# Kernel optimization log

Measured on AMD Instinct MI355X. Metric: run time of the kernel, lower is better.

## Reference

```python
import jax, jax.numpy as jnp
import numpy as np

B, N_HEADS, F_TOK = 8, 12, 768
GRID_H, GRID_W = 32, 32
N_TOK = 1 + GRID_H * GRID_W  # 1025 (readout token + patches)
F_HEAD = F_TOK // N_HEADS    # 64
NUM_DIST = (2 * GRID_H - 1) * (2 * GRID_W - 1) + 3  # 3972


def _build_relpos_index(gh, gw):
    # BEiT-style relative position index with 3 extra slots for the readout token
    coords = np.stack(np.meshgrid(np.arange(gh), np.arange(gw), indexing='ij'))  # (2, gh, gw)
    flat = coords.reshape(2, -1)                                                 # (2, gh*gw)
    rel = flat[:, :, None] - flat[:, None, :]                                    # (2, P, P)
    rel = rel.transpose(1, 2, 0).astype(np.int64)                                # (P, P, 2)
    rel[:, :, 0] += gh - 1
    rel[:, :, 1] += gw - 1
    rel[:, :, 0] *= 2 * gw - 1
    rpi = rel.sum(-1)                                                            # (P, P)
    n = 1 + gh * gw
    nd = (2 * gh - 1) * (2 * gw - 1) + 3
    idx = np.zeros((n, n), dtype=np.int32)
    idx[1:, 1:] = rpi
    idx[0, :] = nd - 3  # readout -> all
    idx[:, 0] = nd - 2  # all -> readout
    idx[0, 0] = nd - 1  # readout -> readout
    return idx


def setup_inputs() -> dict:
    key = jax.random.key(0)
    ks = jax.random.split(key, 7)
    tokens = jax.random.normal(ks[0], (B, N_TOK, F_TOK), dtype=jnp.float32)
    qkv_w = jax.random.normal(ks[1], (3 * F_TOK, F_TOK), dtype=jnp.float32) * 0.02
    q_bias = jax.random.normal(ks[2], (1, N_HEADS, 1, F_HEAD), dtype=jnp.float32) * 0.02
    v_bias = jax.random.normal(ks[3], (1, N_HEADS, 1, F_HEAD), dtype=jnp.float32) * 0.02
    relpos_table = jax.random.normal(ks[4], (NUM_DIST, N_HEADS), dtype=jnp.float32) * 0.02
    proj_w = jax.random.normal(ks[5], (F_TOK, F_TOK), dtype=jnp.float32) * 0.02
    proj_b = jax.random.normal(ks[6], (F_TOK,), dtype=jnp.float32) * 0.02
    relpos_index = jnp.asarray(_build_relpos_index(GRID_H, GRID_W))  # (N, N) int32
    return {
        'tokens': tokens, 'qkv_w': qkv_w, 'q_bias': q_bias, 'v_bias': v_bias,
        'relpos_table': relpos_table, 'proj_w': proj_w, 'proj_b': proj_b,
        'relpos_index': relpos_index, 'patch_h': GRID_H, 'patch_w': GRID_W,
    }


def reference(tokens, qkv_w, q_bias, v_bias, relpos_table, proj_w, proj_b,
              relpos_index, patch_h, patch_w):
    b, n, f_tok = tokens.shape
    # qkv projection (no bias): (B, N, 3F) -> (3, B, H, N, f)
    qkv = tokens @ qkv_w.T
    qkv = qkv.reshape(b, n, 3, N_HEADS, F_HEAD).transpose(2, 0, 3, 1, 4)
    q, k, v = qkv[0], qkv[1], qkv[2]
    q = (q + q_bias) * (F_HEAD ** -0.5)
    v = v + v_bias
    # attention scores: (B, H, N, N)
    attn = jnp.einsum('bhnf,bhmf->bhnm', q, k)
    # relative position bias gather: (N, N, H) -> (H, N, N)
    bias = relpos_table[relpos_index].transpose(2, 0, 1)
    attn = attn + bias[None]
    w = jax.nn.softmax(attn, axis=-1)
    out = jnp.einsum('bhnm,bhmf->bhnf', w, v)
    out = out.transpose(0, 2, 1, 3).reshape(b, n, N_HEADS * F_HEAD)
    return out @ proj_w.T + proj_b
```

## Files before the change

### kernel.cpp

```cpp
#include <hip/hip_runtime.h>

#define B_ 8
#define NH 12
#define NTOK 1025
#define FT 768
#define MROWS (B_*NTOK)
#define QPAD 1025
#define CH2 34
#define NQT 36
#define NTT 34
#define NDIST 3972
#define LOG2E 1.44269504089f

typedef __bf16 bf16x8 __attribute__((ext_vector_type(8)));
typedef __bf16 bf16x2 __attribute__((ext_vector_type(2)));
typedef float floatx4 __attribute__((ext_vector_type(4)));
typedef float floatx16 __attribute__((ext_vector_type(16)));
typedef int intx4 __attribute__((ext_vector_type(4)));

__device__ __forceinline__ void async_ld16(const void* gp, void* lp) {
  __builtin_amdgcn_global_load_lds(
      (const __attribute__((address_space(1))) void*)gp,
      (__attribute__((address_space(3))) void*)lp, 16, 0, 0);
}

__global__ __launch_bounds__(256) void cvt_bf16(const float* __restrict__ src,
                                                __bf16* __restrict__ dst, int n4) {
  int i = blockIdx.x * 256 + threadIdx.x;
  if (i >= n4) return;
  float4 v = ((const float4*)src)[i];
  __bf16 o[4] = {(__bf16)v.x, (__bf16)v.y, (__bf16)v.z, (__bf16)v.w};
  *(uint2*)(dst + 4 * (size_t)i) = *(uint2*)o;
}

__global__ __launch_bounds__(256) void table_prep(const float* __restrict__ table,
                                                  __bf16* __restrict__ tableT) {
  int i = blockIdx.x * 256 + threadIdx.x;
  if (i >= NH * NDIST) return;
  int h = i / NDIST, d = i - h * NDIST;
  tableT[i] = (__bf16)(table[(size_t)d * NH + h] * LOG2E);
}

__global__ __launch_bounds__(256) void bias_gather_t(
    const int* __restrict__ idx, const __bf16* __restrict__ tableT,
    __bf16* __restrict__ Bb) {
  __shared__ int ids_l[32][33];
  const int qt = blockIdx.x, tt = blockIdx.y;
  const int t = threadIdx.x;
  {
    const int row = t >> 3, c4 = (t & 7) * 4;
    int qrow = qt * 32 + row; if (qrow > NTOK - 1) qrow = NTOK - 1;
    const int* src = idx + (size_t)qrow * NTOK;
#pragma unroll
    for (int j = 0; j < 4; ++j) {
      int token = tt * 32 + c4 + j; if (token > NTOK - 1) token = NTOK - 1;
      ids_l[row][c4 + j] = src[token];
    }
  }
  __syncthreads();
  const int lane = t & 63, w = t >> 6;
  const int l31 = lane & 31, hb = lane >> 5;
  int ids[16]; bool ok[16];
#pragma unroll
  for (int j = 0; j < 16; ++j) {
    const int col = (j & 3) + 8 * (j >> 2) + 4 * hb;
    ok[j] = tt * 32 + col < NTOK;
    ids[j] = ids_l[l31][col];
  }
#pragma unroll
  for (int g = 0; g < 3; ++g) {
    const int h = w + g * 4;
    const __bf16* tb = tableT + (size_t)h * NDIST;
    __bf16 v[16] __attribute__((aligned(16)));
#pragma unroll
    for (int j = 0; j < 16; ++j)
      v[j] = ok[j] ? tb[ids[j]] : (__bf16)(-1e30f);
    uint4* dst = (uint4*)(Bb + (((size_t)h * NQT + qt) * NTT + tt) * 1024 + lane * 16);
    dst[0] = ((uint4*)v)[0];
    dst[1] = ((uint4*)v)[1];
  }
}

__device__ __forceinline__ void gemm256_pipe(
    const __bf16* __restrict__ A, const __bf16* __restrict__ W,
    int am0, int n0, __bf16* Lt, floatx4 acc[4][4]) {
  const int tid = threadIdx.x, wave = tid >> 6, lane = tid & 63;
  const int l = lane & 15, qd = lane >> 4;
  const int srow = lane >> 2, sg = lane & 3;
  const int swb = (sg ^ (srow & 3)) * 8;
  const int wr = wave >> 1, wc = wave & 1;

  const __bf16* gsrc[3];
  int gdst[3];
#pragma unroll
  for (int i = 0; i < 3; ++i) {
    const int g = wave * 3 + i;
    if (g < 16) {
      int row = am0 + g * 16 + srow; if (row > MROWS - 1) row = MROWS - 1;
      gsrc[i] = A + (size_t)row * FT + swb;
      gdst[i] = g * 512;
    } else {
      const int row = n0 + (g - 16) * 16 + srow;
      gsrc[i] = W + (size_t)row * FT + swb;
      gdst[i] = 8192 + (g - 16) * 512;
    }
  }
  const int fsw = (qd ^ (l & 3)) * 8;

  auto issue = [&](int k, int buf) {
    __bf16* base = Lt + buf * 12288;
#pragma unroll
    for (int i = 0; i < 3; ++i)
      async_ld16(gsrc[i] + k * 32, base + gdst[i]);
  };
  auto step = [&](int buf) {
    __builtin_amdgcn_s_barrier();
    const __bf16* ab = Lt + buf * 12288;
    const __bf16* bb = ab + 8192;
    bf16x8 aF[4], bF[4];
#pragma unroll
    for (int t = 0; t < 4; ++t)
      aF[t] = *(const bf16x8*)(ab + (wr * 64 + t * 16 + l) * 32 + fsw);
#pragma unroll
    for (int u = 0; u < 4; ++u)
      bF[u] = *(const bf16x8*)(bb + (wc * 64 + u * 16 + l) * 32 + fsw);
#pragma unroll
    for (int t = 0; t < 4; ++t)
#pragma unroll
      for (int u = 0; u < 4; ++u)
        acc[t][u] = __builtin_amdgcn_mfma_f32_16x16x32_bf16(aF[t], bF[u], acc[t][u], 0, 0, 0);
  };

  issue(0, 0);
  int b0 = 0;
  for (int k = 0; k < 24; ++k) {
    if (k < 23) {
      int b1 = b0 + 1; if (b1 == 3) b1 = 0;
      issue(k + 1, b1);
      __builtin_amdgcn_s_waitcnt(0x0F73);
    } else {
      __builtin_amdgcn_s_waitcnt(0x0F70);
    }
    step(b0);
    ++b0; if (b0 == 3) b0 = 0;
  }
}

__global__ __launch_bounds__(512, 4) void qkv_gemm256(
    const __bf16* __restrict__ tokens, const __bf16* __restrict__ qkvw,
    const float* __restrict__ qbias, const float* __restrict__ vbias,
    __bf16* __restrict__ Qb, __bf16* __restrict__ Kc, __bf16* __restrict__ Vc) {
  __shared__ __bf16 Lt[3 * 12288];
  const int u0 = blockIdx.x;
  const int c = u0 & 7, i0 = u0 >> 3;
  const int base = (c < 2) ? c * 75 : 150 + (c - 2) * 74;
  const int w = base + i0;
  const int mt = w / 18, ni = w % 18;
  const int am0 = mt * 256, n0 = ni * 128;
  const int tid = threadIdx.x, wave = tid >> 6, lane = tid & 63;
  const int l = lane & 15, qd = lane >> 4;
  const int wr = wave >> 1, wc = wave & 1;
  floatx4 acc[4][4];
#pragma unroll
  for (int t = 0; t < 4; ++t)
#pragma unroll
    for (int u = 0; u < 4; ++u) acc[t][u] = (floatx4){0.f, 0.f, 0.f, 0.f};
  gemm256_pipe(tokens, qkvw, am0, n0, Lt, acc);

  const int which = ni / 6;
  const int nrem0 = (ni - which * 6) * 128;
#pragma unroll
  for (int u = 0; u < 4; ++u) {
    const int rem = nrem0 + wc * 64 + u * 16 + l;
    const int h = rem >> 6, f = rem & 63;
    const float qb = (which == 0) ? qbias[h * 64 + f] : 0.f;
    const float vb = (which == 2) ? vbias[h * 64 + f] : 0.f;
#pragma unroll
    for (int t = 0; t < 4; ++t) {
      const int gmb = am0 + wr * 64 + t * 16 + qd * 4;
#pragma unroll
      for (int r = 0; r < 4; ++r) {
        const int gm = gmb + r;
        if (gm >= MROWS) continue;
        const int b = (int)(((unsigned)gm * 16369u) >> 24);
        const int tok = gm - b * 1025;
        const size_t bh = (size_t)(b * NH + h);
        const float v = acc[t][u][r];
        if (which == 0) {
          Qb[(bh * QPAD + tok) * 64 + f] = (__bf16)((v + qb) * (0.125f * LOG2E));
        } else if (which == 1) {
          const size_t e = (bh * CH2 + (tok >> 5)) * 2048 +
                           (f >> 3) * 256 + (tok & 31) * 8 + (f & 7);
          Kc[e] = (__bf16)v;
        } else {
          const size_t e = (bh * CH2 + (tok >> 5)) * 2048 +
                           (((tok >> 3) & 3) * 64 + f) * 8 + (tok & 7);
          Vc[e] = (__bf16)(v + vb);
        }
      }
    }
  }
}

__global__ __launch_bounds__(512, 4) void proj_gemm256(
    const __bf16* __restrict__ Ao, const __bf16* __restrict__ projw,
    const float* __restrict__ projb, float* __restrict__ out) {
  __shared__ __bf16 Lt[3 * 12288];
  const int u0 = blockIdx.x;
  const int c = u0 & 7, i0 = u0 >> 3;
  const int base = (c < 6) ? c * 25 : 150 + (c - 6) * 24;
  const int w = base + i0;
  const int mt = w / 6, ni = w % 6;
  const int am0 = mt * 256, n0 = ni * 128;
  const int tid = threadIdx.x, wave = tid >> 6, lane = tid & 63;
  const int l = lane & 15, qd = lane >> 4;
  const int wr = wave >> 1, wc = wave & 1;
  floatx4 acc[4][4];
#pragma unroll
  for (int t = 0; t < 4; ++t)
#pragma unroll
    for (int u = 0; u < 4; ++u) acc[t][u] = (floatx4){0.f, 0.f, 0.f, 0.f};
  gemm256_pipe(Ao, projw, am0, n0, Lt, acc);

#pragma unroll
  for (int u = 0; u < 4; ++u) {
    const int gn = n0 + wc * 64 + u * 16 + l;
    const float pb = projb[gn];
#pragma unroll
    for (int t = 0; t < 4; ++t) {
      const int gmb = am0 + wr * 64 + t * 16 + qd * 4;
#pragma unroll
      for (int r = 0; r < 4; ++r) {
        const int gm = gmb + r;
        if (gm < MROWS) out[(size_t)gm * FT + gn] = acc[t][u][r] + pb;
      }
    }
  }
}

__global__ __launch_bounds__(256) void attn_flash(
    const __bf16* __restrict__ Qb, const __bf16* __restrict__ Kc,
    const __bf16* __restrict__ Vc, const __bf16* __restrict__ Bb,
    __bf16* __restrict__ Ao) {
  __shared__ __bf16 Kl[5][2048], Vl[5][2048];
  const int bh = blockIdx.x;
  const int h = bh % NH, b = bh / NH;
  const int wave = threadIdx.x >> 6, lane = threadIdx.x & 63;
  const int l31 = lane & 31, hb = lane >> 5;
  const int qt = blockIdx.y * 4 + wave;
  int qrow = qt * 32 + l31; if (qrow > NTOK - 1) qrow = NTOK - 1;

  bf16x8 qf[4];
  {
    const __bf16* Qp = Qb + ((size_t)bh * QPAD + qrow) * 64 + hb * 8;
#pragma unroll
    for (int d = 0; d < 4; ++d) qf[d] = *(const bf16x8*)(Qp + d * 16);
  }

  floatx16 o0, o1;
#pragma unroll
  for (int j = 0; j < 16; ++j) { o0[j] = 0.f; o1[j] = 0.f; }
  float lsum = 0.f;

  const int sw = wave & 1;
  const __bf16* Sg = ((wave < 2) ? Kc : Vc) + (size_t)bh * CH2 * 2048 +
                     sw * 1024 + lane * 8;
  __bf16* Sl0 = ((wave < 2) ? &Kl[0][0] : &Vl[0][0]) + sw * 1024;
  const __bf16* Bg = Bb + ((size_t)h * NQT + qt) * NTT * 1024 + lane * 16;

  auto issueS = [&](int c, int buf) {
    const __bf16* src = Sg + (size_t)c * 2048;
    __bf16* dst = Sl0 + buf * 2048;
    async_ld16(src, dst);
    async_ld16(src + 512, dst + 512);
  };

  auto compute = [&](int buf, bf16x8 cb0, bf16x8 cb1) {
    const __bf16* Kb = &Kl[buf][0];
    const __bf16* Vb = &Vl[buf][0];
    floatx16 st;
#pragma unroll
    for (int j = 0; j < 16; ++j) st[j] = 0.f;
#pragma unroll
    for (int dk = 0; dk < 4; ++dk) {
      bf16x8 a = *(const bf16x8*)(Kb + ((dk * 2 + hb) * 32 + l31) * 8);
      st = __builtin_amdgcn_mfma_f32_32x32x16_bf16(a, qf[dk], st, 0, 0, 0);
    }
    float e[16];
#pragma unroll
    for (int j = 0; j < 16; ++j) {
      const float bj = (float)(j < 8 ? cb0[j] : cb1[j - 8]);
      e[j] = __builtin_amdgcn_exp2f(st[j] + bj);
      lsum += e[j];
    }
    int pk[8];
#pragma unroll
    for (int j2 = 0; j2 < 8; ++j2) {
      bf16x2 pr = {(__bf16)e[2 * j2], (__bf16)e[2 * j2 + 1]};
      pk[j2] = __builtin_bit_cast(int, pr);
    }
#pragma unroll
    for (int ks = 0; ks < 2; ++ks) {
      const int r01a = pk[4 * ks + 0], r01b = pk[4 * ks + 1];
      const int r23a = pk[4 * ks + 2], r23b = pk[4 * ks + 3];
      const int t01a = __shfl_xor(r01a, 32), t01b = __shfl_xor(r01b, 32);
      const int t23a = __shfl_xor(r23a, 32), t23b = __shfl_xor(r23b, 32);
      intx4 fi;
      fi[0] = hb ? t23a : r01a;
      fi[1] = hb ? t23b : r01b;
      fi[2] = hb ? r23a : t01a;
      fi[3] = hb ? r23b : t01b;
      bf16x8 pb = __builtin_bit_cast(bf16x8, fi);
      bf16x8 va0 = *(const bf16x8*)(Vb + ((ks * 2 + hb) * 64 + l31) * 8);
      bf16x8 va1 = *(const bf16x8*)(Vb + ((ks * 2 + hb) * 64 + 32 + l31) * 8);
      o0 = __builtin_amdgcn_mfma_f32_32x32x16_bf16(va0, pb, o0, 0, 0, 0);
      o1 = __builtin_amdgcn_mfma_f32_32x32x16_bf16(va1, pb, o1, 0, 0, 0);
    }
  };

  issueS(0, 0);
  bf16x8 bA0 = *(const bf16x8*)(Bg);
  bf16x8 bA1 = *(const bf16x8*)(Bg + 8);
  issueS(1, 1);
  bf16x8 bB0 = *(const bf16x8*)(Bg + 1024);
  bf16x8 bB1 = *(const bf16x8*)(Bg + 1024 + 8);
  issueS(2, 2);

  int bc = 0;
  for (int ci = 0; ci < 15; ++ci) {
    const int c = 2 * ci;
    __builtin_amdgcn_s_waitcnt(0x0F76);
    __builtin_amdgcn_s_barrier();
    compute(bc, bA0, bA1);
    bA0 = *(const bf16x8*)(Bg + (size_t)(c + 2) * 1024);
    bA1 = *(const bf16x8*)(Bg + (size_t)(c + 2) * 1024 + 8);
    { int b3 = bc + 3; if (b3 >= 5) b3 -= 5; issueS(c + 3, b3); }
    int bc1 = bc + 1; if (bc1 == 5) bc1 = 0;
    __builtin_amdgcn_s_waitcnt(0x0F76);
    __builtin_amdgcn_s_barrier();
    compute(bc1, bB0, bB1);
    bB0 = *(const bf16x8*)(Bg + (size_t)(c + 3) * 1024);
    bB1 = *(const bf16x8*)(Bg + (size_t)(c + 3) * 1024 + 8);
    { int b4 = bc + 4; if (b4 >= 5) b4 -= 5; issueS(c + 4, b4); }
    bc += 2; if (bc >= 5) bc -= 5;
  }
  __builtin_amdgcn_s_waitcnt(0x0F76);
  __builtin_amdgcn_s_barrier();
  compute(0, bA0, bA1);
  bA0 = *(const bf16x8*)(Bg + (size_t)32 * 1024);
  bA1 = *(const bf16x8*)(Bg + (size_t)32 * 1024 + 8);
  issueS(33, 3);
  __builtin_amdgcn_s_waitcnt(0x0F76);
  __builtin_amdgcn_s_barrier();
  compute(1, bB0, bB1);
  bB0 = *(const bf16x8*)(Bg + (size_t)33 * 1024);
  bB1 = *(const bf16x8*)(Bg + (size_t)33 * 1024 + 8);
  __builtin_amdgcn_s_waitcnt(0x0F74);
  __builtin_amdgcn_s_barrier();
  compute(2, bA0, bA1);
  __builtin_amdgcn_s_waitcnt(0x0F70);
  __builtin_amdgcn_s_barrier();
  compute(3, bB0, bB1);

  const float ltot = lsum + __shfl_xor(lsum, 32);
  const float rinv = 1.0f / ltot;
  const int tok = qt * 32 + l31;
  if (tok < NTOK) {
    __bf16* op = Ao + ((size_t)b * NTOK + tok) * FT + h * 64;
#pragma unroll
    for (int ft = 0; ft < 2; ++ft) {
#pragma unroll
      for (int jg = 0; jg < 4; ++jg) {
        const int f = ft * 32 + jg * 8 + hb * 4;
        __bf16 v4[4] __attribute__((aligned(8)));
#pragma unroll
        for (int q = 0; q < 4; ++q) {
          const float ov = ft ? o1[jg * 4 + q] : o0[jg * 4 + q];
          v4[q] = (__bf16)(ov * rinv);
        }
        *(uint2*)(op + f) = *(uint2*)v4;
      }
    }
  }
}

extern "C" void kernel_launch(void* const* d_in, const int* in_sizes, int n_in,
                              void* d_out, int out_size, void* d_ws, size_t ws_size,
                              hipStream_t stream) {
  (void)in_sizes; (void)n_in; (void)out_size; (void)ws_size;
  const float* tokens = (const float*)d_in[0];
  const float* qkvw   = (const float*)d_in[1];
  const float* qbias  = (const float*)d_in[2];
  const float* vbias  = (const float*)d_in[3];
  const float* table  = (const float*)d_in[4];
  const float* projw  = (const float*)d_in[5];
  const float* projb  = (const float*)d_in[6];
  const int*   rpidx  = (const int*)d_in[7];
  float* out = (float*)d_out;
  char* ws = (char*)d_ws;

  const size_t QBQ = (size_t)B_ * NH * QPAD * 64 * 2;
  const size_t KVB = (size_t)B_ * NH * CH2 * 2048 * 2;
  const size_t BBT = (size_t)NH * NQT * NTT * 1024 * 2;
  const size_t AOB = (size_t)MROWS * FT * 2;
  const size_t WQB = (size_t)3 * FT * FT * 2;
  const size_t WPB = (size_t)FT * FT * 2;
  __bf16* Qb = (__bf16*)(ws);
  __bf16* Kc = (__bf16*)(ws + QBQ);
  __bf16* Vc = (__bf16*)(ws + QBQ + KVB);
  __bf16* Bb = (__bf16*)(ws + QBQ + 2 * KVB);
  __bf16* Tb = (__bf16*)(ws + QBQ + 2 * KVB + BBT);
  __bf16* Ao = Tb;
  __bf16* Wq = (__bf16*)(ws + QBQ + 2 * KVB + BBT + AOB);
  __bf16* Wp = (__bf16*)(ws + QBQ + 2 * KVB + BBT + AOB + WQB);
  __bf16* Tt = (__bf16*)(ws + QBQ + 2 * KVB + BBT + AOB + WQB + WPB);

  cvt_bf16<<<(MROWS * FT / 4 + 255) / 256, 256, 0, stream>>>(tokens, Tb, MROWS * FT / 4);
  cvt_bf16<<<(3 * FT * FT / 4 + 255) / 256, 256, 0, stream>>>(qkvw, Wq, 3 * FT * FT / 4);
  cvt_bf16<<<(FT * FT / 4 + 255) / 256, 256, 0, stream>>>(projw, Wp, FT * FT / 4);
  table_prep<<<(NH * NDIST + 255) / 256, 256, 0, stream>>>(table, Tt);
  bias_gather_t<<<dim3(NQT, NTT), 256, 0, stream>>>(rpidx, Tt, Bb);
  qkv_gemm256<<<33 * 18, 512, 0, stream>>>(Tb, Wq, qbias, vbias, Qb, Kc, Vc);
  attn_flash<<<dim3(B_ * NH, 9), 256, 0, stream>>>(Qb, Kc, Vc, Bb, Ao);
  proj_gemm256<<<33 * 6, 512, 0, stream>>>(Ao, Wp, projb, out);
}
```

Measured before the change: 246.7 us.

## Process 64-key tiles per stage with triple buffering and split QK/SV phases

The attention loop now handles two 32-key tiles per pipeline stage, using a 3-deep LDS ring of 4096-element K/V buffers instead of a 5-deep ring of 2048-element buffers. The bias is folded into the MFMA accumulator init, prefetch is issued between the QK and PV phases, and s_setprio hints are wrapped around the MFMA sections. The aim is to halve the barrier count and interleave exp work with MFMA across waves. A launch-bounds occupancy hint of 3 blocks is added, which may constrain registers given the doubled score accumulators.

```diff
diff --git a/kernel.cpp b/kernel.cpp
--- a/kernel.cpp
+++ b/kernel.cpp
@@ -238,11 +238,11 @@
   }
 }
 
-__global__ __launch_bounds__(256) void attn_flash(
+__global__ __launch_bounds__(256, 3) void attn_flash(
     const __bf16* __restrict__ Qb, const __bf16* __restrict__ Kc,
     const __bf16* __restrict__ Vc, const __bf16* __restrict__ Bb,
     __bf16* __restrict__ Ao) {
-  __shared__ __bf16 Kl[5][2048], Vl[5][2048];
+  __shared__ __bf16 Kl[3][4096], Vl[3][4096];
   const int bh = blockIdx.x;
   const int h = bh % NH, b = bh / NH;
   const int wave = threadIdx.x >> 6, lane = threadIdx.x & 63;
@@ -260,109 +260,123 @@
   floatx16 o0, o1;
 #pragma unroll
   for (int j = 0; j < 16; ++j) { o0[j] = 0.f; o1[j] = 0.f; }
-  float lsum = 0.f;
+  float lsA = 0.f, lsB = 0.f;
 
   const int sw = wave & 1;
   const __bf16* Sg = ((wave < 2) ? Kc : Vc) + (size_t)bh * CH2 * 2048 +
-                     sw * 1024 + lane * 8;
-  __bf16* Sl0 = ((wave < 2) ? &Kl[0][0] : &Vl[0][0]) + sw * 1024;
+                     sw * 2048 + lane * 8;
+  __bf16* Sl0 = ((wave < 2) ? &Kl[0][0] : &Vl[0][0]) + sw * 2048;
   const __bf16* Bg = Bb + ((size_t)h * NQT + qt) * NTT * 1024 + lane * 16;
 
-  auto issueS = [&](int c, int buf) {
-    const __bf16* src = Sg + (size_t)c * 2048;
-    __bf16* dst = Sl0 + buf * 2048;
+  auto issueS = [&](int c2, int buf) {
+    const __bf16* src = Sg + (size_t)c2 * 4096;
+    __bf16* dst = Sl0 + buf * 4096;
     async_ld16(src, dst);
     async_ld16(src + 512, dst + 512);
-  };
-
-  auto compute = [&](int buf, bf16x8 cb0, bf16x8 cb1) {
+    async_ld16(src + 1024, dst + 1024);
+    async_ld16(src + 1536, dst + 1536);
+  };
+
+  bf16x8 bA0, bA1, bA2, bA3, bB0, bB1, bB2, bB3;
+  auto loadBA = [&](int c2) {
+    const __bf16* p = Bg + (size_t)(2 * c2) * 1024;
+    bA0 = *(const bf16x8*)(p);
+    bA1 = *(const bf16x8*)(p + 8);
+    bA2 = *(const bf16x8*)(p + 1024);
+    bA3 = *(const bf16x8*)(p + 1032);
+  };
+  auto loadBB = [&](int c2) {
+    const __bf16* p = Bg + (size_t)(2 * c2) * 1024;
+    bB0 = *(const bf16x8*)(p);
+    bB1 = *(const bf16x8*)(p + 8);
+    bB2 = *(const bf16x8*)(p + 1024);
+    bB3 = *(const bf16x8*)(p + 1032);
+  };
+
+  floatx16 st0, st1;
+  auto qkPart = [&](int buf, bf16x8 c0, bf16x8 c1, bf16x8 c2, bf16x8 c3) {
     const __bf16* Kb = &Kl[buf][0];
-    const __bf16* Vb = &Vl[buf][0];
-    floatx16 st;
-#pragma unroll
-    for (int j = 0; j < 16; ++j) st[j] = 0.f;
+#pragma unroll
+    for (int j = 0; j < 16; ++j) {
+      st0[j] = (float)(j < 8 ? c0[j] : c1[j - 8]);
+      st1[j] = (float)(j < 8 ? c2[j] : c3[j - 8]);
+    }
+    __builtin_amdgcn_s_setprio(1);
 #pragma unroll
     for (int dk = 0; dk < 4; ++dk) {
-      bf16x8 a = *(const bf16x8*)(Kb + ((dk * 2 + hb) * 32 + l31) * 8);
-      st = __builtin_amdgcn_mfma_f32_32x32x16_bf16(a, qf[dk], st, 0, 0, 0);
-    }
-    float e[16];
-#pragma unroll
-    for (int j = 0; j < 16; ++j) {
-      const float bj = (float)(j < 8 ? cb0[j] : cb1[j - 8]);
-      e[j] = __builtin_amdgcn_exp2f(st[j] + bj);
-      lsum += e[j];
-    }
-    int pk[8];
-#pragma unroll
-    for (int j2 = 0; j2 < 8; ++j2) {
-      bf16x2 pr = {(__bf16)e[2 * j2], (__bf16)e[2 * j2 + 1]};
-      pk[j2] = __builtin_bit_cast(int, pr);
-    }
-#pragma unroll
-    for (int ks = 0; ks < 2; ++ks) {
-      const int r01a = pk[4 * ks + 0], r01b = pk[4 * ks + 1];
-      const int r23a = pk[4 * ks + 2], r23b = pk[4 * ks + 3];
-      const int t01a = __shfl_xor(r01a, 32), t01b = __shfl_xor(r01b, 32);
-      const int t23a = __shfl_xor(r23a, 32), t23b = __shfl_xor(r23b, 32);
-      intx4 fi;
-      fi[0] = hb ? t23a : r01a;
-      fi[1] = hb ? t23b : r01b;
-      fi[2] = hb ? r23a : t01a;
-      fi[3] = hb ? r23b : t01b;
-      bf16x8 pb = __builtin_bit_cast(bf16x8, fi);
-      bf16x8 va0 = *(const bf16x8*)(Vb + ((ks * 2 + hb) * 64 + l31) * 8);
-      bf16x8 va1 = *(const bf16x8*)(Vb + ((ks * 2 + hb) * 64 + 32 + l31) * 8);
-      o0 = __builtin_amdgcn_mfma_f32_32x32x16_bf16(va0, pb, o0, 0, 0, 0);
-      o1 = __builtin_amdgcn_mfma_f32_32x32x16_bf16(va1, pb, o1, 0, 0, 0);
+      bf16x8 a0 = *(const bf16x8*)(Kb + ((dk * 2 + hb) * 32 + l31) * 8);
+      bf16x8 a1 = *(const bf16x8*)(Kb + 2048 + ((dk * 2 + hb) * 32 + l31) * 8);
+      st0 = __builtin_amdgcn_mfma_f32_32x32x16_bf16(a0, qf[dk], st0, 0, 0, 0);
+      st1 = __builtin_amdgcn_mfma_f32_32x32x16_bf16(a1, qf[dk], st1, 0, 0, 0);
+    }
+    __builtin_amdgcn_s_setprio(0);
+  };
+
+  auto svPart = [&](int buf) {
+#pragma unroll
+    for (int th = 0; th < 2; ++th) {
+      const floatx16& st = th ? st1 : st0;
+      const __bf16* Vb = &Vl[buf][0] + th * 2048;
+      float e[16];
+#pragma unroll
+      for (int j = 0; j < 16; ++j) e[j] = __builtin_amdgcn_exp2f(st[j]);
+      lsA += ((e[0] + e[1]) + (e[2] + e[3])) + ((e[4] + e[5]) + (e[6] + e[7]));
+      lsB += ((e[8] + e[9]) + (e[10] + e[11])) + ((e[12] + e[13]) + (e[14] + e[15]));
+      int pk[8];
+#pragma unroll
+      for (int j2 = 0; j2 < 8; ++j2) {
+        bf16x2 pr = {(__bf16)e[2 * j2], (__bf16)e[2 * j2 + 1]};
+        pk[j2] = __builtin_bit_cast(int, pr);
+      }
+      __builtin_amdgcn_s_setprio(1);
+#pragma unroll
+      for (int ks = 0; ks < 2; ++ks) {
+        const int r01a = pk[4 * ks + 0], r01b = pk[4 * ks + 1];
+        const int r23a = pk[4 * ks + 2], r23b = pk[4 * ks + 3];
+        const int t01a = __shfl_xor(r01a, 32), t01b = __shfl_xor(r01b, 32);
+        const int t23a = __shfl_xor(r23a, 32), t23b = __shfl_xor(r23b, 32);
+        intx4 fi;
+        fi[0] = hb ? t23a : r01a;
+        fi[1] = hb ? t23b : r01b;
+        fi[2] = hb ? r23a : t01a;
+        fi[3] = hb ? r23b : t01b;
+        bf16x8 pb = __builtin_bit_cast(bf16x8, fi);
+        bf16x8 va0 = *(const bf16x8*)(Vb + ((ks * 2 + hb) * 64 + l31) * 8);
+        bf16x8 va1 = *(const bf16x8*)(Vb + ((ks * 2 + hb) * 64 + 32 + l31) * 8);
+        o0 = __builtin_amdgcn_mfma_f32_32x32x16_bf16(va0, pb, o0, 0, 0, 0);
+        o1 = __builtin_amdgcn_mfma_f32_32x32x16_bf16(va1, pb, o1, 0, 0, 0);
+      }
+      __builtin_amdgcn_s_setprio(0);
     }
   };
 
   issueS(0, 0);
-  bf16x8 bA0 = *(const bf16x8*)(Bg);
-  bf16x8 bA1 = *(const bf16x8*)(Bg + 8);
+  loadBA(0);
   issueS(1, 1);
-  bf16x8 bB0 = *(const bf16x8*)(Bg + 1024);
-  bf16x8 bB1 = *(const bf16x8*)(Bg + 1024 + 8);
-  issueS(2, 2);
-
-  int bc = 0;
-  for (int ci = 0; ci < 15; ++ci) {
+  loadBB(1);
+  int bufc = 0;
+  for (int ci = 0; ci < 8; ++ci) {
     const int c = 2 * ci;
-    __builtin_amdgcn_s_waitcnt(0x0F76);
+    __builtin_amdgcn_s_waitcnt(0x0F78);
     __builtin_amdgcn_s_barrier();
-    compute(bc, bA0, bA1);
-    bA0 = *(const bf16x8*)(Bg + (size_t)(c + 2) * 1024);
-    bA1 = *(const bf16x8*)(Bg + (size_t)(c + 2) * 1024 + 8);
-    { int b3 = bc + 3; if (b3 >= 5) b3 -= 5; issueS(c + 3, b3); }
-    int bc1 = bc + 1; if (bc1 == 5) bc1 = 0;
-    __builtin_amdgcn_s_waitcnt(0x0F76);
+    qkPart(bufc, bA0, bA1, bA2, bA3);
+    { int pb_ = bufc + 2; if (pb_ >= 3) pb_ -= 3; issueS(c + 2, pb_); loadBA(c + 2); }
+    svPart(bufc);
+    bufc = (bufc + 1 == 3) ? 0 : bufc + 1;
+    __builtin_amdgcn_s_waitcnt(0x0F78);
     __builtin_amdgcn_s_barrier();
-    compute(bc1, bB0, bB1);
-    bB0 = *(const bf16x8*)(Bg + (size_t)(c + 3) * 1024);
-    bB1 = *(const bf16x8*)(Bg + (size_t)(c + 3) * 1024 + 8);
-    { int b4 = bc + 4; if (b4 >= 5) b4 -= 5; issueS(c + 4, b4); }
-    bc += 2; if (bc >= 5) bc -= 5;
-  }
-  __builtin_amdgcn_s_waitcnt(0x0F76);
-  __builtin_amdgcn_s_barrier();
-  compute(0, bA0, bA1);
-  bA0 = *(const bf16x8*)(Bg + (size_t)32 * 1024);
-  bA1 = *(const bf16x8*)(Bg + (size_t)32 * 1024 + 8);
-  issueS(33, 3);
-  __builtin_amdgcn_s_waitcnt(0x0F76);
-  __builtin_amdgcn_s_barrier();
-  compute(1, bB0, bB1);
-  bB0 = *(const bf16x8*)(Bg + (size_t)33 * 1024);
-  bB1 = *(const bf16x8*)(Bg + (size_t)33 * 1024 + 8);
-  __builtin_amdgcn_s_waitcnt(0x0F74);
-  __builtin_amdgcn_s_barrier();
-  compute(2, bA0, bA1);
+    qkPart(bufc, bB0, bB1, bB2, bB3);
+    if (ci < 7) { int pb_ = bufc + 2; if (pb_ >= 3) pb_ -= 3; issueS(c + 3, pb_); loadBB(c + 3); }
+    svPart(bufc);
+    bufc = (bufc + 1 == 3) ? 0 : bufc + 1;
+  }
   __builtin_amdgcn_s_waitcnt(0x0F70);
   __builtin_amdgcn_s_barrier();
-  compute(3, bB0, bB1);
-
-  const float ltot = lsum + __shfl_xor(lsum, 32);
+  qkPart(bufc, bA0, bA1, bA2, bA3);
+  svPart(bufc);
+
+  const float ls = lsA + lsB;
+  const float ltot = ls + __shfl_xor(ls, 32);
   const float rinv = 1.0f / ltot;
   const int tok = qt * 32 + l31;
   if (tok < NTOK) {
```

Measured after the change: 314.5 us. 27.5% more time.
